# Kernel optimization log

Measured on AMD Instinct MI355X. Metric: run time of the kernel, lower is better.

The kernel has to match this reference:

```python
import math
import jax, jax.numpy as jnp
import numpy as np

Q_MAX = 127.0  # 2**(8-1) - 1 for n_bits=8
SCALE_EPS = 1e-5


def _hadamard_matrix(n):
    H = np.array([[1.0]], dtype=np.float32)
    while H.shape[0] < n:
        H = np.block([[H, H], [H, -H]])
    return jnp.asarray(H)


def quantize_per_channel_absmax(w):
    # per output-channel absmax quantize-dequantize (torch weight per_channel)
    scales = jnp.clip(jnp.max(jnp.abs(w), axis=-1, keepdims=True) / Q_MAX, SCALE_EPS, None)
    return jnp.round(w / scales) * scales


def quantize_per_token_absmax(x):
    # per-token (last-dim) absmax quantize-dequantize
    scales = jnp.clip(jnp.max(jnp.abs(x), axis=-1, keepdims=True) / Q_MAX, SCALE_EPS, None)
    return jnp.round(x / scales) * scales


def setup_inputs() -> dict:
    key = jax.random.key(0)
    k1, k2, k3 = jax.random.split(key, 3)
    B, S, D_IN, D_OUT = 2, 2048, 4096, 4096
    x = jax.random.normal(k1, (B, S, D_IN), dtype=jnp.float32)
    # weight quantized at __init__ time (per_channel, 8-bit), as in the wrapper
    weight = quantize_per_channel_absmax(
        jax.random.normal(k2, (D_OUT, D_IN), dtype=jnp.float32) * (1.0 / math.sqrt(D_IN)))
    bias = jax.random.normal(k3, (D_OUT,), dtype=jnp.float32)
    return {"x": x, "weight": weight, "bias": bias, "had_dim": 64}


def reference(x, weight, bias, had_dim):
    # --- online_partial_had, K == 1 path ---
    B, S, D = x.shape
    n_groups = D // had_dim
    H = _hadamard_matrix(n_groups).astype(x.dtype)
    xr = x.reshape(-1, n_groups, had_dim)  # (B*S, G, had_dim)
    # hadamard_transform along the group axis, scale = 1/sqrt(G)
    xr = jnp.einsum('hg,bgd->bhd', H, xr) * (1.0 / math.sqrt(n_groups))
    x = xr.reshape(B, S, D)
    # --- per-token absmax activation quant ---
    x = quantize_per_token_absmax(x)
    # --- linear with (already quantized) weight ---
    return jnp.einsum('bsd,od->bso', x, weight) + bias
```

## Files before the change

kernel.cpp:

```cpp
#include <hip/hip_runtime.h>
#include <hip/hip_bf16.h>

#define M_DIM 4096
#define N_DIM 4096
#define K_DIM 4096

typedef __attribute__((ext_vector_type(4))) int i32x4;
typedef __attribute__((ext_vector_type(16))) int i32x16;

typedef __attribute__((address_space(1))) const void GV;
typedef __attribute__((address_space(3))) void LV;

__global__ __launch_bounds__(256) void prequant_kernel(const float* __restrict__ x,
                                                       const float* __restrict__ w,
                                                       char* __restrict__ xq,
                                                       char* __restrict__ wq,
                                                       float* __restrict__ sx,
                                                       float* __restrict__ sw) {
  const int wave = threadIdx.x >> 6;
  const int lane = threadIdx.x & 63;

  if (blockIdx.x >= 1024) {
    const int row = (blockIdx.x - 1024) * 4 + wave;
    const float* wp = w + (size_t)row * 4096;
    float4 v[16];
#pragma unroll
    for (int c = 0; c < 16; ++c) v[c] = *(const float4*)(wp + c * 256 + lane * 4);
    float amax = 0.f;
#pragma unroll
    for (int c = 0; c < 16; ++c)
      amax = fmaxf(amax, fmaxf(fmaxf(fabsf(v[c].x), fabsf(v[c].y)),
                               fmaxf(fabsf(v[c].z), fabsf(v[c].w))));
#pragma unroll
    for (int off = 32; off >= 1; off >>= 1) amax = fmaxf(amax, __shfl_xor(amax, off, 64));
    amax = fmaxf(amax, 1e-30f);
    const float inv = 127.0f / amax;
    char* op = wq + (size_t)row * 4096;
#pragma unroll
    for (int c = 0; c < 16; ++c) {
      char4 o;
      o.x = (char)rintf(v[c].x * inv);
      o.y = (char)rintf(v[c].y * inv);
      o.z = (char)rintf(v[c].z * inv);
      o.w = (char)rintf(v[c].w * inv);
      *(char4*)(op + c * 256 + lane * 4) = o;
    }
    if (lane == 0) sw[row] = amax * (1.0f / 127.0f);
    return;
  }

  const int tok = blockIdx.x * 4 + wave;
  const int gs = lane >> 4;
  const int q = lane & 15;
  const float* xp = x + (size_t)tok * 4096;

  float4 v[16];
#pragma unroll
  for (int gl = 0; gl < 16; ++gl)
    v[gl] = *(const float4*)(xp + (gl * 4 + gs) * 64 + q * 4);

#pragma unroll
  for (int s = 1; s < 16; s <<= 1) {
#pragma unroll
    for (int i = 0; i < 16; ++i) {
      if ((i & s) == 0) {
        float4 a = v[i], b = v[i | s];
        v[i].x = a.x + b.x; v[i].y = a.y + b.y; v[i].z = a.z + b.z; v[i].w = a.w + b.w;
        v[i | s].x = a.x - b.x; v[i | s].y = a.y - b.y;
        v[i | s].z = a.z - b.z; v[i | s].w = a.w - b.w;
      }
    }
  }
#pragma unroll
  for (int st = 0; st < 2; ++st) {
    const int L = 16 << st;
    const bool hi = (lane & L) != 0;
#pragma unroll
    for (int i = 0; i < 16; ++i) {
      float4 t;
      t.x = __shfl_xor(v[i].x, L, 64);
      t.y = __shfl_xor(v[i].y, L, 64);
      t.z = __shfl_xor(v[i].z, L, 64);
      t.w = __shfl_xor(v[i].w, L, 64);
      if (hi) {
        v[i].x = t.x - v[i].x; v[i].y = t.y - v[i].y;
        v[i].z = t.z - v[i].z; v[i].w = t.w - v[i].w;
      } else {
        v[i].x += t.x; v[i].y += t.y; v[i].z += t.z; v[i].w += t.w;
      }
    }
  }

  float amax = 0.f;
#pragma unroll
  for (int i = 0; i < 16; ++i) {
    v[i].x *= 0.125f; v[i].y *= 0.125f; v[i].z *= 0.125f; v[i].w *= 0.125f;
    amax = fmaxf(amax, fmaxf(fmaxf(fabsf(v[i].x), fabsf(v[i].y)),
                             fmaxf(fabsf(v[i].z), fabsf(v[i].w))));
  }
#pragma unroll
  for (int off = 32; off >= 1; off >>= 1) amax = fmaxf(amax, __shfl_xor(amax, off, 64));

  const float s = fmaxf(amax * (1.0f / 127.0f), 1e-5f);
  const float inv = 1.0f / s;

  char* op = xq + (size_t)tok * 4096;
#pragma unroll
  for (int gl = 0; gl < 16; ++gl) {
    char4 o;
    o.x = (char)rintf(v[gl].x * inv);
    o.y = (char)rintf(v[gl].y * inv);
    o.z = (char)rintf(v[gl].z * inv);
    o.w = (char)rintf(v[gl].w * inv);
    *(char4*)(op + (gl * 4 + gs) * 64 + q * 4) = o;
  }
  if (lane == 0) sx[tok] = s;
}

__global__ __launch_bounds__(256, 3) void gemm_i8(const char* __restrict__ A,
                                                  const char* __restrict__ B,
                                                  const float* __restrict__ sx,
                                                  const float* __restrict__ sw,
                                                  const float* __restrict__ bias,
                                                  float* __restrict__ C) {
  __shared__ char As[128 * 128];
  __shared__ char Bs[128 * 128];

  const int tid = threadIdx.x;
  const int lane = tid & 63;
  const int wave = tid >> 6;
  const int bm = blockIdx.y, bn = blockIdx.x;
  const int wm = wave >> 1, wn = wave & 1;

  const int trow = tid >> 3;
  const int tseg = (tid & 7) ^ (trow & 7);
  const char* gA = A + (size_t)(bm * 128 + trow) * K_DIM + tseg * 16;
  const char* gB = B + (size_t)(bn * 128 + trow) * K_DIM + tseg * 16;
  char* lA = &As[tid * 16];
  char* lB = &Bs[tid * 16];

  const int m32 = lane & 31;
  const int half = lane >> 5;
  const int aBase = (wm * 64 + m32) * 128;
  const int bBase = (wn * 64 + m32) * 128;
  int sl[4];
#pragma unroll
  for (int kc = 0; kc < 4; ++kc) sl[kc] = ((kc * 2 + half) ^ (m32 & 7)) * 16;

  i32x16 acc[2][2];
#pragma unroll
  for (int i = 0; i < 2; ++i)
#pragma unroll
    for (int j = 0; j < 2; ++j)
#pragma unroll
      for (int r = 0; r < 16; ++r) acc[i][j][r] = 0;

  for (int kt = 0; kt < K_DIM / 128; ++kt) {
    __syncthreads();
    const size_t ke = (size_t)kt * 128;
#pragma unroll
    for (int c = 0; c < 4; ++c) {
      __builtin_amdgcn_global_load_lds((GV*)(gA + ke + (size_t)c * 32 * K_DIM),
                                       (LV*)(lA + c * 4096), 16, 0, 0);
      __builtin_amdgcn_global_load_lds((GV*)(gB + ke + (size_t)c * 32 * K_DIM),
                                       (LV*)(lB + c * 4096), 16, 0, 0);
    }
    __syncthreads();

#pragma unroll
    for (int kc = 0; kc < 4; ++kc) {
      i32x4 a0 = *(const i32x4*)&As[aBase + sl[kc]];
      i32x4 a1 = *(const i32x4*)&As[aBase + 4096 + sl[kc]];
      i32x4 b0 = *(const i32x4*)&Bs[bBase + sl[kc]];
      i32x4 b1 = *(const i32x4*)&Bs[bBase + 4096 + sl[kc]];
      acc[0][0] = __builtin_amdgcn_mfma_i32_32x32x32_i8(a0, b0, acc[0][0], 0, 0, 0);
      acc[0][1] = __builtin_amdgcn_mfma_i32_32x32x32_i8(a0, b1, acc[0][1], 0, 0, 0);
      acc[1][0] = __builtin_amdgcn_mfma_i32_32x32x32_i8(a1, b0, acc[1][0], 0, 0, 0);
      acc[1][1] = __builtin_amdgcn_mfma_i32_32x32x32_i8(a1, b1, acc[1][1], 0, 0, 0);
    }
  }

  float swv[2], bv[2];
#pragma unroll
  for (int j = 0; j < 2; ++j) {
    const int colg = bn * 128 + wn * 64 + j * 32 + m32;
    swv[j] = sw[colg];
    bv[j] = bias[colg];
  }

#pragma unroll
  for (int i = 0; i < 2; ++i) {
    const int rbase = bm * 128 + wm * 64 + i * 32 + 4 * half;
    float sxv[16];
#pragma unroll
    for (int r = 0; r < 16; ++r) sxv[r] = sx[rbase + (r & 3) + 8 * (r >> 2)];
#pragma unroll
    for (int j = 0; j < 2; ++j) {
      const int colg = bn * 128 + wn * 64 + j * 32 + m32;
#pragma unroll
      for (int r = 0; r < 16; ++r) {
        const int rowg = rbase + (r & 3) + 8 * (r >> 2);
        C[(size_t)rowg * N_DIM + colg] = (float)acc[i][j][r] * (sxv[r] * swv[j]) + bv[j];
      }
    }
  }
}

extern "C" void kernel_launch(void* const* d_in, const int* in_sizes, int n_in,
                              void* d_out, int out_size, void* d_ws, size_t ws_size,
                              hipStream_t stream) {
  const float* x = (const float*)d_in[0];
  const float* w = (const float*)d_in[1];
  const float* bias = (const float*)d_in[2];

  char* xq = (char*)d_ws;
  char* wq = xq + (size_t)M_DIM * K_DIM;
  float* sx = (float*)(wq + (size_t)N_DIM * K_DIM);
  float* sw = sx + M_DIM;
  float* out = (float*)d_out;

  prequant_kernel<<<2048, 256, 0, stream>>>(x, w, xq, wq, sx, sw);

  dim3 grid(N_DIM / 128, M_DIM / 128);
  gemm_i8<<<grid, 256, 0, stream>>>(xq, wq, sx, sw, bias, out);
}
```

Baseline: 247.7 us.

## Double-buffer LDS tiles in int8 GEMM to overlap loads with MFMA

The int8 GEMM now keeps two LDS buffers for the A and B tiles. It issues the async global-to-LDS load for the next K tile before running the MFMAs on the current one, so memory latency can hide behind compute instead of stalling between two barriers. LDS use per block doubles to 64KB, and the launch-bounds occupancy hint drops from 3 to 2 blocks per CU, which lowers parallelism between waves.

```diff
diff --git a/kernel.cpp b/kernel.cpp
--- a/kernel.cpp
+++ b/kernel.cpp
@@ -117,14 +117,14 @@
   if (lane == 0) sx[tok] = s;
 }
 
-__global__ __launch_bounds__(256, 3) void gemm_i8(const char* __restrict__ A,
+__global__ __launch_bounds__(256, 2) void gemm_i8(const char* __restrict__ A,
                                                   const char* __restrict__ B,
                                                   const float* __restrict__ sx,
                                                   const float* __restrict__ sw,
                                                   const float* __restrict__ bias,
                                                   float* __restrict__ C) {
-  __shared__ char As[128 * 128];
-  __shared__ char Bs[128 * 128];
+  __shared__ char As[2][128 * 128];
+  __shared__ char Bs[2][128 * 128];
 
   const int tid = threadIdx.x;
   const int lane = tid & 63;
@@ -136,8 +136,7 @@
   const int tseg = (tid & 7) ^ (trow & 7);
   const char* gA = A + (size_t)(bm * 128 + trow) * K_DIM + tseg * 16;
   const char* gB = B + (size_t)(bn * 128 + trow) * K_DIM + tseg * 16;
-  char* lA = &As[tid * 16];
-  char* lB = &Bs[tid * 16];
+  const int ldst = tid * 16;
 
   const int m32 = lane & 31;
   const int half = lane >> 5;
@@ -155,29 +154,40 @@
 #pragma unroll
       for (int r = 0; r < 16; ++r) acc[i][j][r] = 0;
 
-  for (int kt = 0; kt < K_DIM / 128; ++kt) {
-    __syncthreads();
+  auto stage = [&](int kt, int b) {
     const size_t ke = (size_t)kt * 128;
 #pragma unroll
     for (int c = 0; c < 4; ++c) {
       __builtin_amdgcn_global_load_lds((GV*)(gA + ke + (size_t)c * 32 * K_DIM),
-                                       (LV*)(lA + c * 4096), 16, 0, 0);
+                                       (LV*)(&As[b][ldst + c * 4096]), 16, 0, 0);
       __builtin_amdgcn_global_load_lds((GV*)(gB + ke + (size_t)c * 32 * K_DIM),
-                                       (LV*)(lB + c * 4096), 16, 0, 0);
-    }
-    __syncthreads();
-
+                                       (LV*)(&Bs[b][ldst + c * 4096]), 16, 0, 0);
+    }
+  };
+
+  auto compute = [&](int b) {
 #pragma unroll
     for (int kc = 0; kc < 4; ++kc) {
-      i32x4 a0 = *(const i32x4*)&As[aBase + sl[kc]];
-      i32x4 a1 = *(const i32x4*)&As[aBase + 4096 + sl[kc]];
-      i32x4 b0 = *(const i32x4*)&Bs[bBase + sl[kc]];
-      i32x4 b1 = *(const i32x4*)&Bs[bBase + 4096 + sl[kc]];
+      i32x4 a0 = *(const i32x4*)&As[b][aBase + sl[kc]];
+      i32x4 a1 = *(const i32x4*)&As[b][aBase + 4096 + sl[kc]];
+      i32x4 b0 = *(const i32x4*)&Bs[b][bBase + sl[kc]];
+      i32x4 b1 = *(const i32x4*)&Bs[b][bBase + 4096 + sl[kc]];
       acc[0][0] = __builtin_amdgcn_mfma_i32_32x32x32_i8(a0, b0, acc[0][0], 0, 0, 0);
       acc[0][1] = __builtin_amdgcn_mfma_i32_32x32x32_i8(a0, b1, acc[0][1], 0, 0, 0);
       acc[1][0] = __builtin_amdgcn_mfma_i32_32x32x32_i8(a1, b0, acc[1][0], 0, 0, 0);
       acc[1][1] = __builtin_amdgcn_mfma_i32_32x32x32_i8(a1, b1, acc[1][1], 0, 0, 0);
     }
+  };
+
+  stage(0, 0);
+  const int NT = K_DIM / 128;
+  for (int kt = 0; kt < NT; kt += 2) {
+    __syncthreads();
+    if (kt + 1 < NT) stage(kt + 1, 1);
+    compute(0);
+    __syncthreads();
+    if (kt + 2 < NT) stage(kt + 2, 0);
+    compute(1);
   }
 
   float swv[2], bv[2];
```

Result: no change. 249.1 us (+0.6%).
